# Optimization experiments

Hardware: AMD Instinct MI355X
Metric: run time of the kernel (lower is better)

Reference implementation:

```python
import jax, jax.numpy as jnp
import numpy as np

# spk_param = (thr, temp, damp); dt, tau from module config
THR, TEMP, DAMP = 0.4, 0.1, 0.9
DT, TAU = 0.1, 1.0


@jax.custom_vjp
def spike(v, u):
    # Stochastic Bernoulli spike: sigmoid(temp*v) > uniform noise
    return (jax.nn.sigmoid(TEMP * v) > u).astype(v.dtype)

def _spike_fwd(v, u):
    return spike(v, u), v

def _spike_bwd(v, g):
    # Faithful to the torch Spike.backward: returns the pseudo-derivative
    # damp*clamp(1-|v|,0) directly (the original ignores grad_output).
    return (DAMP * jnp.maximum(1.0 - jnp.abs(v), 0.0), jnp.zeros_like(v))

spike.defvjp(_spike_fwd, _spike_bwd)


def setup_inputs() -> dict:
    key = jax.random.key(0)
    k1, k2, k3, k4, k5 = jax.random.split(key, 5)
    B_, T, IN, N, OUT = 128, 512, 128, 512, 128
    inputs = jax.random.normal(k1, (B_, T, IN), dtype=jnp.float32)
    rand_u = jax.random.uniform(k2, (B_, T, N), dtype=jnp.float32)
    init_std = 1.0
    J = jax.random.normal(k3, (N, N), dtype=jnp.float32) * (init_std / np.sqrt(N))
    Bw = jax.random.normal(k4, (N, IN), dtype=jnp.float32)  # input projection (non-trainable in torch)
    W = jax.random.normal(k5, (OUT, N), dtype=jnp.float32) * (1.0 / np.sqrt(N))
    return {"inputs": inputs, "rand_u": rand_u, "J": J, "Bw": Bw, "W": W}


def reference(inputs, rand_u, J, Bw, W):
    B_, T, _ = inputs.shape
    N = J.shape[0]
    alpha = DT / TAU
    decay = 1.0 - alpha

    def step(carry, xs):
        v, z = carry
        x_t, u_t = xs  # [B, IN], [B, N]
        v_new = decay * v + alpha * z
        lamb = jnp.tanh(v_new) @ J.T + x_t @ Bw.T  # [B, N]
        z_new = spike((lamb - THR) / THR, u_t)
        out = lamb @ W.T  # [B, OUT]
        return (v_new, z_new), (v_new, z_new, out)

    v0 = jnp.zeros((B_, N), dtype=inputs.dtype)
    z0 = jnp.zeros((B_, N), dtype=inputs.dtype)
    xs = (jnp.swapaxes(inputs, 0, 1), jnp.swapaxes(rand_u, 0, 1))  # time-major
    _, (vs, zs, outs) = jax.lax.scan(step, (v0, z0), xs)

    vt = jnp.concatenate([v0[:, None, :], jnp.swapaxes(vs, 0, 1)], axis=1)  # [B, T+1, N]
    zt = jnp.concatenate([z0[:, None, :], jnp.swapaxes(zs, 0, 1)], axis=1)  # [B, T+1, N]
    output_seq = jnp.swapaxes(outs, 0, 1)  # [B, T, OUT]
    return vt, zt, output_seq
```

## Files before the change

### kernel.cpp

```cpp
#include <hip/hip_runtime.h>


typedef __attribute__((ext_vector_type(8))) short short8x;
typedef __attribute__((ext_vector_type(4))) float f32x4;

#define OFF_JQK  (0u)
#define OFF_BWH  (262144u)
#define OFF_BWL  (393216u)
#define OFF_G    (524288u)
#define OFF_M    (786432u)
#define OFF_GPK  (851968u)
#define OFF_MPK  (983040u)

#define SC_J 640.0f
#define SC_S 166.0f

__device__ __forceinline__ unsigned short f2bf(float f) {
  union { float f; unsigned u; } a; a.f = f;
  unsigned r = a.u + 0x7FFFu + ((a.u >> 16) & 1u);
  return (unsigned short)(r >> 16);
}
__device__ __forceinline__ float bf2f(unsigned short h) {
  union { unsigned u; float f; } a; a.u = ((unsigned)h) << 16;
  return a.f;
}
__device__ __forceinline__ float thr_of(float u) {
  return __builtin_fmaf(4.0f, __logf(u / (1.0f - u)), 0.4f);
}
__device__ __forceinline__ float fast_tanh_pos(float x) {
  const float e2 = __expf(x + x);
  return 1.0f - 2.0f / (e2 + 1.0f);
}
__device__ __forceinline__ int sdot4(unsigned a, unsigned b, int acc) {
#if __has_builtin(__builtin_amdgcn_sdot4)
  return __builtin_amdgcn_sdot4((int)a, (int)b, acc, false);
#else
  int r;
  asm("v_dot4_i32_i8 %0, %1, %2, %3" : "=v"(r) : "v"(a), "v"(b), "v"(acc));
  return r;
#endif
}
template <int CTRL>
__device__ __forceinline__ int dpp_add(int x) {
  return x + __builtin_amdgcn_update_dpp(0, x, CTRL, 0xF, 0xF, true);
}
__device__ __forceinline__ int dpp_reduce8(int x) {
  return dpp_add<0x141>(dpp_add<0x4E>(dpp_add<0xB1>(x)));
}

__launch_bounds__(512)
__global__ void jwm_kernel(const float* __restrict__ J, const float* __restrict__ Bw,
                           const float* __restrict__ W, unsigned char* __restrict__ ws) {
  __shared__ float wrow[512];
  const int o = blockIdx.x;
  const int tid = threadIdx.x;
  wrow[tid] = W[(size_t)o * 512 + tid];
  __syncthreads();
  const int k = tid, i = tid & 127;
  float g = 0.0f, m = 0.0f;
  for (int n = 0; n < 512; ++n) {
    const float wv = wrow[n];
    g = __builtin_fmaf(wv, J[(size_t)n * 512 + k], g);
    m = __builtin_fmaf(wv, Bw[(size_t)n * 128 + i], m);
  }
  ((float*)(ws + OFF_G))[(size_t)o * 512 + k] = g;
  if (tid < 128) ((float*)(ws + OFF_M))[(size_t)o * 128 + i] = m;
}

__global__ void pack_kernel(const float* __restrict__ J, const float* __restrict__ Bw,
                            unsigned char* __restrict__ ws) {
  const int id = blockIdx.x * 256 + threadIdx.x;
  if (id < 16384) {
    const int f = id;
    const int l = f & 63, j = (f >> 6) & 3, i = (f >> 8) & 7, w = f >> 11;
    const int kap = l & 7;
    const int n = w * 64 + (l >> 3) * 8 + i;
    const int k0 = 64 * kap + 16 * j;
    unsigned dw[4];
#pragma unroll
    for (int d = 0; d < 4; ++d) {
      unsigned x = 0;
#pragma unroll
      for (int p = 0; p < 4; ++p) {
        const float jv = J[(size_t)n * 512 + k0 + 4 * d + p];
        int q = __float2int_rn(jv * SC_J);
        q = q > 127 ? 127 : (q < -127 ? -127 : q);
        x |= ((unsigned)(q & 255)) << (8 * p);
      }
      dw[d] = x;
    }
    uint4 out; out.x = dw[0]; out.y = dw[1]; out.z = dw[2]; out.w = dw[3];
    ((uint4*)(ws + OFF_JQK))[f] = out;
  } else if (id < 24576) {
    const int idx = id - 16384;
    const int n = idx & 511, kg = idx >> 9, k0 = kg * 8;
    unsigned short* bwh = (unsigned short*)(ws + OFF_BWH);
    unsigned short* bwl = (unsigned short*)(ws + OFF_BWL);
    for (int e = 0; e < 8; ++e) {
      const float x = Bw[(size_t)n * 128 + k0 + e];
      const unsigned short h = f2bf(x);
      bwh[(size_t)idx * 8 + e] = h;
      bwl[(size_t)idx * 8 + e] = f2bf(x - bf2f(h));
    }
  } else if (id < 32768) {
    const int idx = id - 24576;
    const int o = idx & 127, kg = idx >> 7, k0 = kg * 8;
    const float* G = (const float*)(ws + OFF_G);
    unsigned short* gpk = (unsigned short*)(ws + OFF_GPK);
    for (int e = 0; e < 8; ++e) gpk[(size_t)idx * 8 + e] = f2bf(G[(size_t)o * 512 + k0 + e]);
  } else {
    const int idx = id - 32768;
    const int o = idx & 127, kg = idx >> 7, k0 = kg * 8;
    const float* M = (const float*)(ws + OFF_M);
    unsigned short* mpk = (unsigned short*)(ws + OFF_MPK);
    for (int e = 0; e < 8; ++e) mpk[(size_t)idx * 8 + e] = f2bf(M[(size_t)o * 128 + k0 + e]);
  }
}

__launch_bounds__(256)
__global__ void xpd_kernel(const float* __restrict__ X, const float* __restrict__ U,
                           const unsigned char* __restrict__ ws, float* __restrict__ Dbuf) {
  __shared__ short Ah[64 * 136];
  __shared__ short Al[64 * 136];
  const unsigned short* bwh = (const unsigned short*)(ws + OFF_BWH);
  const unsigned short* bwl = (const unsigned short*)(ws + OFF_BWL);
  const int m0 = blockIdx.x * 64;
  const int n0 = blockIdx.y * 64;
  const int tid = threadIdx.x;
  for (int i = tid; i < 64 * 32; i += 256) {
    const int r = i >> 5, kq = i & 31;
    const float4 x4 = *(const float4*)(X + (size_t)(m0 + r) * 128 + kq * 4);
    short4 h4, l4; unsigned short h;
    h = f2bf(x4.x); h4.x = (short)h; l4.x = (short)f2bf(x4.x - bf2f(h));
    h = f2bf(x4.y); h4.y = (short)h; l4.y = (short)f2bf(x4.y - bf2f(h));
    h = f2bf(x4.z); h4.z = (short)h; l4.z = (short)f2bf(x4.z - bf2f(h));
    h = f2bf(x4.w); h4.w = (short)h; l4.w = (short)f2bf(x4.w - bf2f(h));
    *(short4*)(&Ah[r * 136 + kq * 4]) = h4;
    *(short4*)(&Al[r * 136 + kq * 4]) = l4;
  }
  __syncthreads();
  const int w = tid >> 6, l = tid & 63, lhi = l >> 4, llo = l & 15;
  const int rowA = 16 * w + llo;
  f32x4 a0 = {0,0,0,0}, a1 = {0,0,0,0}, a2 = {0,0,0,0}, a3 = {0,0,0,0};
#pragma unroll
  for (int kt = 0; kt < 4; ++kt) {
    const short8x ah = *(const short8x*)(&Ah[rowA * 136 + kt * 32 + lhi * 8]);
    const short8x al = *(const short8x*)(&Al[rowA * 136 + kt * 32 + lhi * 8]);
#define XT(TI, ACC) { \
    const size_t bi = ((size_t)((kt * 4 + lhi) * 512 + n0 + TI * 16 + llo)) * 8; \
    const short8x bh = *(const short8x*)(bwh + bi); \
    const short8x bl = *(const short8x*)(bwl + bi); \
    ACC = __builtin_amdgcn_mfma_f32_16x16x32_bf16(ah, bh, ACC, 0, 0, 0); \
    ACC = __builtin_amdgcn_mfma_f32_16x16x32_bf16(al, bh, ACC, 0, 0, 0); \
    ACC = __builtin_amdgcn_mfma_f32_16x16x32_bf16(ah, bl, ACC, 0, 0, 0); }
    XT(0, a0) XT(1, a1) XT(2, a2) XT(3, a3)
#undef XT
  }
  const int n = n0 + llo;
#pragma unroll
  for (int r = 0; r < 4; ++r) {
    const int bt = m0 + 16 * w + lhi * 4 + r;
    const int bb = bt >> 9, tt = bt & 511;
    const float* urow = U + (size_t)bt * 512;
    float* drow = Dbuf + ((size_t)bb * 513 + tt + 1) * 512;
    drow[n]      = thr_of(urow[n])      - a0[r];
    drow[n + 16] = thr_of(urow[n + 16]) - a1[r];
    drow[n + 32] = thr_of(urow[n + 32]) - a2[r];
    drow[n + 48] = thr_of(urow[n + 48]) - a3[r];
  }
}

__launch_bounds__(512, 1)
__global__ void recur_kernel(const unsigned char* __restrict__ ws,
                             const float* __restrict__ Dv,
                             float* __restrict__ vtw, float* __restrict__ ztw) {
  __shared__ __align__(16) unsigned char s_sm[2][640];
  const int b = blockIdx.x;
  const int tid = threadIdx.x;
  const int w = tid >> 6, l = tid & 63;
  const int kap = l & 7, kap80 = kap * 80;

  uint4 jr[8][4];
#pragma unroll
  for (int i = 0; i < 8; ++i)
#pragma unroll
    for (int j = 0; j < 4; ++j) {
      const unsigned char* p = ws + OFF_JQK +
          (size_t)(((w * 8 + i) * 4 + j) * 64 + l) * 16;
      asm volatile("global_load_dwordx4 %0, %1, off" : "=v"(jr[i][j]) : "v"(p));
    }
  asm volatile("s_waitcnt vmcnt(0)" ::: "memory");

  const float SC = 1.0f / (SC_J * SC_S);
  vtw[((size_t)b * 513) * 512 + tid] = 0.0f;
  ztw[((size_t)b * 513) * 512 + tid] = 0.0f;

  const float* Dp = Dv + ((size_t)b * 513 + 1) * 512 + tid;
  float* vbase = vtw + ((size_t)b * 513 + 1) * 512 + tid;
  float* zbase = ztw + ((size_t)b * 513 + 1) * 512 + tid;

  float dc[8], dnx[8];
#pragma unroll
  for (int i = 0; i < 8; ++i) dc[i] = Dp[(size_t)i * 512];

  unsigned zprev = 0u;
  float v0 = 0.0f, v1 = 0.1f;
  unsigned q0 = (unsigned)__float2int_rn(fast_tanh_pos(v0) * SC_S);
  unsigned q1 = (unsigned)__float2int_rn(fast_tanh_pos(v1) * SC_S);

  for (int c = 0; c < 64; ++c) {
    const int t0 = c * 8;
#pragma unroll
    for (int i = 0; i < 8; ++i) dnx[i] = Dp[(size_t)(t0 + 8 + i) * 512];
    float v_arr[8];
    unsigned zbits = 0u;
#pragma unroll
    for (int i = 0; i < 8; ++i) {
      const int t = t0 + i;
      const unsigned q = zprev ? q1 : q0;
      const float v = zprev ? v1 : v0;
      v_arr[i] = v;
      s_sm[t & 1][w * 80 + l] = (unsigned char)q;
      asm volatile("s_waitcnt lgkmcnt(0)\n\ts_barrier" ::: "memory");
      v0 = 0.9f * v; v1 = v0 + 0.1f;
      q0 = (unsigned)__float2int_rn(fast_tanh_pos(v0) * SC_S);
      q1 = (unsigned)__float2int_rn(fast_tanh_pos(v1) * SC_S);
      const unsigned char* sb = &s_sm[t & 1][0];
      const uint4 s0 = *(const uint4*)(sb + kap80);
      const uint4 s1 = *(const uint4*)(sb + kap80 + 16);
      const uint4 s2 = *(const uint4*)(sb + kap80 + 32);
      const uint4 s3 = *(const uint4*)(sb + kap80 + 48);
      int a0 = 0, a1 = 0, a2 = 0, a3 = 0, a4 = 0, a5 = 0, a6 = 0, a7 = 0;
#define DOT(AI, I) \
      AI = sdot4(jr[I][0].x, s0.x, AI); AI = sdot4(jr[I][0].y, s0.y, AI); \
      AI = sdot4(jr[I][0].z, s0.z, AI); AI = sdot4(jr[I][0].w, s0.w, AI); \
      AI = sdot4(jr[I][1].x, s1.x, AI); AI = sdot4(jr[I][1].y, s1.y, AI); \
      AI = sdot4(jr[I][1].z, s1.z, AI); AI = sdot4(jr[I][1].w, s1.w, AI); \
      AI = sdot4(jr[I][2].x, s2.x, AI); AI = sdot4(jr[I][2].y, s2.y, AI); \
      AI = sdot4(jr[I][2].z, s2.z, AI); AI = sdot4(jr[I][2].w, s2.w, AI); \
      AI = sdot4(jr[I][3].x, s3.x, AI); AI = sdot4(jr[I][3].y, s3.y, AI); \
      AI = sdot4(jr[I][3].z, s3.z, AI); AI = sdot4(jr[I][3].w, s3.w, AI);
      DOT(a0, 0) DOT(a1, 1) DOT(a2, 2) DOT(a3, 3)
      DOT(a4, 4) DOT(a5, 5) DOT(a6, 6) DOT(a7, 7)
#undef DOT
      a0 = dpp_reduce8(a0); a1 = dpp_reduce8(a1);
      a2 = dpp_reduce8(a2); a3 = dpp_reduce8(a3);
      a4 = dpp_reduce8(a4); a5 = dpp_reduce8(a5);
      a6 = dpp_reduce8(a6); a7 = dpp_reduce8(a7);
      const int q01 = (l & 1) ? a1 : a0;
      const int q23 = (l & 1) ? a3 : a2;
      const int q45 = (l & 1) ? a5 : a4;
      const int q67 = (l & 1) ? a7 : a6;
      const int r0 = (l & 2) ? q23 : q01;
      const int r1 = (l & 2) ? q67 : q45;
      const int accv = (l & 4) ? r1 : r0;
      const float lam = (float)accv * SC;
      const unsigned z = (lam > dc[i]) ? 1u : 0u;
      zbits |= z << i;
      zprev = z;
    }
    unsigned zzero;
    asm("v_and_b32 %0, 0, %1" : "=v"(zzero) : "v"(zprev));
    float* vst = vbase + (size_t)t0 * 512 + zzero;
    float* zst = zbase + (size_t)t0 * 512;
#pragma unroll
    for (int i = 0; i < 8; ++i) {
      vst[(size_t)i * 512] = v_arr[i];
      zst[(size_t)i * 512] = ((zbits >> i) & 1u) ? 1.0f : 0.0f;
    }
#pragma unroll
    for (int i = 0; i < 8; ++i) dc[i] = dnx[i];
  }
}

__launch_bounds__(512)
__global__ void outk_kernel(const float* __restrict__ X, const float* __restrict__ vt,
                            const unsigned char* __restrict__ ws,
                            float* __restrict__ op) {
  __shared__ unsigned short sl[64 * 520];
  __shared__ unsigned short xl[64 * 136];
  const int m0 = blockIdx.x * 64;
  const int tid = threadIdx.x;
  const int w = tid >> 6, l = tid & 63, lhi = l >> 4, llo = l & 15;
  const unsigned short* gpk = (const unsigned short*)(ws + OFF_GPK);
  const unsigned short* mpk = (const unsigned short*)(ws + OFF_MPK);

#pragma unroll 4
  for (int r = 0; r < 64; ++r) {
    const int bt = m0 + r, b = bt >> 9, t = bt & 511;
    const float v = vt[((size_t)b * 513 + t + 1) * 512 + tid];
    sl[r * 520 + tid] = f2bf(fast_tanh_pos(v));
  }
#pragma unroll
  for (int i = 0; i < 16; ++i) {
    const int idx = i * 512 + tid;
    const int r = idx >> 7, c = idx & 127;
    const int bt = m0 + r;
    xl[r * 136 + c] = f2bf(X[(size_t)bt * 128 + c]);
  }
  __syncthreads();
  const int m = w >> 1, oh = (w & 1) * 4;
  f32x4 a0 = {0,0,0,0}, a1 = {0,0,0,0}, a2 = {0,0,0,0}, a3 = {0,0,0,0};
#pragma unroll
  for (int kt = 0; kt < 16; ++kt) {
    const short8x A = *(const short8x*)(sl + (m * 16 + llo) * 520 + kt * 32 + lhi * 8);
#define GT(TI, ACC) { \
    const short8x B = *(const short8x*)(gpk + ((size_t)((kt * 4 + lhi) * 128 + (oh + TI) * 16 + llo)) * 8); \
    ACC = __builtin_amdgcn_mfma_f32_16x16x32_bf16(A, B, ACC, 0, 0, 0); }
    GT(0, a0) GT(1, a1) GT(2, a2) GT(3, a3)
#undef GT
  }
#pragma unroll
  for (int kt = 0; kt < 4; ++kt) {
    const short8x A = *(const short8x*)(xl + (m * 16 + llo) * 136 + kt * 32 + lhi * 8);
#define MT(TI, ACC) { \
    const short8x B = *(const short8x*)(mpk + ((size_t)((kt * 4 + lhi) * 128 + (oh + TI) * 16 + llo)) * 8); \
    ACC = __builtin_amdgcn_mfma_f32_16x16x32_bf16(A, B, ACC, 0, 0, 0); }
    MT(0, a0) MT(1, a1) MT(2, a2) MT(3, a3)
#undef MT
  }
  float* obase = op + ((size_t)(m0 + m * 16 + lhi * 4)) * 128 + llo;
#pragma unroll
  for (int r = 0; r < 4; ++r) {
    float* orow = obase + (size_t)r * 128;
    orow[(oh + 0) * 16] = a0[r];
    orow[(oh + 1) * 16] = a1[r];
    orow[(oh + 2) * 16] = a2[r];
    orow[(oh + 3) * 16] = a3[r];
  }
}

extern "C" void kernel_launch(void* const* d_in, const int* in_sizes, int n_in,
                              void* d_out, int out_size, void* d_ws, size_t ws_size,
                              hipStream_t stream) {
  const float* X  = (const float*)d_in[0];
  const float* U  = (const float*)d_in[1];
  const float* J  = (const float*)d_in[2];
  const float* Bw = (const float*)d_in[3];
  const float* W  = (const float*)d_in[4];
  float* vt = (float*)d_out;
  float* zt = vt + (size_t)128 * 513 * 512;
  float* op = vt + (size_t)2 * 128 * 513 * 512;
  unsigned char* ws = (unsigned char*)d_ws;

  jwm_kernel<<<128, 512, 0, stream>>>(J, Bw, W, ws);
  pack_kernel<<<136, 256, 0, stream>>>(J, Bw, ws);
  xpd_kernel<<<dim3(1024, 8), 256, 0, stream>>>(X, U, ws, vt);
  recur_kernel<<<128, 512, 0, stream>>>(ws, vt, vt, zt);
  outk_kernel<<<1024, 512, 0, stream>>>(X, vt, ws, op);
}
```

Measured before the change: 680.5 us.

## Split recurrent int8 dot over 16 lanes with 1024-thread blocks

The recurrence kernel now runs 1024 threads per batch row instead of 512. Each neuron's J row is split across 16 lanes rather than 8, so each lane holds half the J registers and does half the sdot4 work per step, with an extra DPP stage in the reduction. The J packing layout is changed to match, duplicate lanes split the v and z stores between them, and next-step D loads are issued inline. The aim is to shorten the serial per-timestep critical path. The cost is a barrier across 16 waves instead of 8 and redundant spike computation in the duplicate lanes.

```diff
diff --git a/kernel.cpp b/kernel.cpp
--- a/kernel.cpp
+++ b/kernel.cpp
@@ -44,8 +44,8 @@
 __device__ __forceinline__ int dpp_add(int x) {
   return x + __builtin_amdgcn_update_dpp(0, x, CTRL, 0xF, 0xF, true);
 }
-__device__ __forceinline__ int dpp_reduce8(int x) {
-  return dpp_add<0x141>(dpp_add<0x4E>(dpp_add<0xB1>(x)));
+__device__ __forceinline__ int dpp_reduce16(int x) {
+  return dpp_add<0x140>(dpp_add<0x141>(dpp_add<0x4E>(dpp_add<0xB1>(x))));
 }
 
 __launch_bounds__(512)
@@ -72,10 +72,10 @@
   const int id = blockIdx.x * 256 + threadIdx.x;
   if (id < 16384) {
     const int f = id;
-    const int l = f & 63, j = (f >> 6) & 3, i = (f >> 8) & 7, w = f >> 11;
-    const int kap = l & 7;
-    const int n = w * 64 + (l >> 3) * 8 + i;
-    const int k0 = 64 * kap + 16 * j;
+    const int l = f & 63, j = (f >> 6) & 1, i = (f >> 7) & 7, w = f >> 10;
+    const int kap = l & 15;
+    const int n = w * 32 + (l >> 4) * 8 + i;
+    const int k0 = 32 * kap + 16 * j;
     unsigned dw[4];
 #pragma unroll
     for (int d = 0; d < 4; ++d) {
@@ -170,7 +170,7 @@
   }
 }
 
-__launch_bounds__(512, 1)
+__launch_bounds__(1024)
 __global__ void recur_kernel(const unsigned char* __restrict__ ws,
                              const float* __restrict__ Dv,
                              float* __restrict__ vtw, float* __restrict__ ztw) {
@@ -178,28 +178,33 @@
   const int b = blockIdx.x;
   const int tid = threadIdx.x;
   const int w = tid >> 6, l = tid & 63;
-  const int kap = l & 7, kap80 = kap * 80;
-
-  uint4 jr[8][4];
+  const int kap = l & 15;
+  const int n_own = w * 32 + (l >> 4) * 8 + (l & 7);
+  const int sm_wr = (n_own >> 6) * 80 + (n_own & 63);
+  const int roff = (kap >> 1) * 80 + (kap & 1) * 32;
+
+  uint4 jr[8][2];
 #pragma unroll
   for (int i = 0; i < 8; ++i)
 #pragma unroll
-    for (int j = 0; j < 4; ++j) {
+    for (int j = 0; j < 2; ++j) {
       const unsigned char* p = ws + OFF_JQK +
-          (size_t)(((w * 8 + i) * 4 + j) * 64 + l) * 16;
+          (size_t)(((w * 8 + i) * 2 + j) * 64 + l) * 16;
       asm volatile("global_load_dwordx4 %0, %1, off" : "=v"(jr[i][j]) : "v"(p));
     }
   asm volatile("s_waitcnt vmcnt(0)" ::: "memory");
 
   const float SC = 1.0f / (SC_J * SC_S);
-  vtw[((size_t)b * 513) * 512 + tid] = 0.0f;
-  ztw[((size_t)b * 513) * 512 + tid] = 0.0f;
-
-  const float* Dp = Dv + ((size_t)b * 513 + 1) * 512 + tid;
-  float* vbase = vtw + ((size_t)b * 513 + 1) * 512 + tid;
-  float* zbase = ztw + ((size_t)b * 513 + 1) * 512 + tid;
-
-  float dc[8], dnx[8];
+  if (tid < 512) {
+    vtw[((size_t)b * 513) * 512 + tid] = 0.0f;
+    ztw[((size_t)b * 513) * 512 + tid] = 0.0f;
+  }
+
+  const float* Dp = Dv + ((size_t)b * 513 + 1) * 512 + n_own;
+  float* vbase = vtw + ((size_t)b * 513 + 1) * 512 + n_own;
+  float* zbase = ztw + ((size_t)b * 513 + 1) * 512 + n_own;
+
+  float dc[8];
 #pragma unroll
   for (int i = 0; i < 8; ++i) dc[i] = Dp[(size_t)i * 512];
 
@@ -210,8 +215,6 @@
 
   for (int c = 0; c < 64; ++c) {
     const int t0 = c * 8;
-#pragma unroll
-    for (int i = 0; i < 8; ++i) dnx[i] = Dp[(size_t)(t0 + 8 + i) * 512];
     float v_arr[8];
     unsigned zbits = 0u;
 #pragma unroll
@@ -220,33 +223,27 @@
       const unsigned q = zprev ? q1 : q0;
       const float v = zprev ? v1 : v0;
       v_arr[i] = v;
-      s_sm[t & 1][w * 80 + l] = (unsigned char)q;
+      if (!(l & 8)) s_sm[t & 1][sm_wr] = (unsigned char)q;
       asm volatile("s_waitcnt lgkmcnt(0)\n\ts_barrier" ::: "memory");
       v0 = 0.9f * v; v1 = v0 + 0.1f;
       q0 = (unsigned)__float2int_rn(fast_tanh_pos(v0) * SC_S);
       q1 = (unsigned)__float2int_rn(fast_tanh_pos(v1) * SC_S);
       const unsigned char* sb = &s_sm[t & 1][0];
-      const uint4 s0 = *(const uint4*)(sb + kap80);
-      const uint4 s1 = *(const uint4*)(sb + kap80 + 16);
-      const uint4 s2 = *(const uint4*)(sb + kap80 + 32);
-      const uint4 s3 = *(const uint4*)(sb + kap80 + 48);
+      const uint4 s0 = *(const uint4*)(sb + roff);
+      const uint4 s1 = *(const uint4*)(sb + roff + 16);
       int a0 = 0, a1 = 0, a2 = 0, a3 = 0, a4 = 0, a5 = 0, a6 = 0, a7 = 0;
 #define DOT(AI, I) \
       AI = sdot4(jr[I][0].x, s0.x, AI); AI = sdot4(jr[I][0].y, s0.y, AI); \
       AI = sdot4(jr[I][0].z, s0.z, AI); AI = sdot4(jr[I][0].w, s0.w, AI); \
       AI = sdot4(jr[I][1].x, s1.x, AI); AI = sdot4(jr[I][1].y, s1.y, AI); \
-      AI = sdot4(jr[I][1].z, s1.z, AI); AI = sdot4(jr[I][1].w, s1.w, AI); \
-      AI = sdot4(jr[I][2].x, s2.x, AI); AI = sdot4(jr[I][2].y, s2.y, AI); \
-      AI = sdot4(jr[I][2].z, s2.z, AI); AI = sdot4(jr[I][2].w, s2.w, AI); \
-      AI = sdot4(jr[I][3].x, s3.x, AI); AI = sdot4(jr[I][3].y, s3.y, AI); \
-      AI = sdot4(jr[I][3].z, s3.z, AI); AI = sdot4(jr[I][3].w, s3.w, AI);
+      AI = sdot4(jr[I][1].z, s1.z, AI); AI = sdot4(jr[I][1].w, s1.w, AI);
       DOT(a0, 0) DOT(a1, 1) DOT(a2, 2) DOT(a3, 3)
       DOT(a4, 4) DOT(a5, 5) DOT(a6, 6) DOT(a7, 7)
 #undef DOT
-      a0 = dpp_reduce8(a0); a1 = dpp_reduce8(a1);
-      a2 = dpp_reduce8(a2); a3 = dpp_reduce8(a3);
-      a4 = dpp_reduce8(a4); a5 = dpp_reduce8(a5);
-      a6 = dpp_reduce8(a6); a7 = dpp_reduce8(a7);
+      a0 = dpp_reduce16(a0); a1 = dpp_reduce16(a1);
+      a2 = dpp_reduce16(a2); a3 = dpp_reduce16(a3);
+      a4 = dpp_reduce16(a4); a5 = dpp_reduce16(a5);
+      a6 = dpp_reduce16(a6); a7 = dpp_reduce16(a7);
       const int q01 = (l & 1) ? a1 : a0;
       const int q23 = (l & 1) ? a3 : a2;
       const int q45 = (l & 1) ? a5 : a4;
@@ -258,18 +255,19 @@
       const unsigned z = (lam > dc[i]) ? 1u : 0u;
       zbits |= z << i;
       zprev = z;
+      dc[i] = Dp[(size_t)(t0 + 8 + i) * 512];
     }
     unsigned zzero;
     asm("v_and_b32 %0, 0, %1" : "=v"(zzero) : "v"(zprev));
-    float* vst = vbase + (size_t)t0 * 512 + zzero;
-    float* zst = zbase + (size_t)t0 * 512;
-#pragma unroll
-    for (int i = 0; i < 8; ++i) {
-      vst[(size_t)i * 512] = v_arr[i];
-      zst[(size_t)i * 512] = ((zbits >> i) & 1u) ? 1.0f : 0.0f;
-    }
-#pragma unroll
-    for (int i = 0; i < 8; ++i) dc[i] = dnx[i];
+    if (!(l & 8)) {
+      float* vst = vbase + (size_t)t0 * 512 + zzero;
+#pragma unroll
+      for (int i = 0; i < 8; ++i) vst[(size_t)i * 512] = v_arr[i];
+    } else {
+      float* zst = zbase + (size_t)t0 * 512 + zzero;
+#pragma unroll
+      for (int i = 0; i < 8; ++i) zst[(size_t)i * 512] = ((zbits >> i) & 1u) ? 1.0f : 0.0f;
+    }
   }
 }
 
@@ -346,6 +344,6 @@
   jwm_kernel<<<128, 512, 0, stream>>>(J, Bw, W, ws);
   pack_kernel<<<136, 256, 0, stream>>>(J, Bw, ws);
   xpd_kernel<<<dim3(1024, 8), 256, 0, stream>>>(X, U, ws, vt);
-  recur_kernel<<<128, 512, 0, stream>>>(ws, vt, vt, zt);
+  recur_kernel<<<128, 1024, 0, stream>>>(ws, vt, vt, zt);
   outk_kernel<<<1024, 512, 0, stream>>>(X, vt, ws, op);
 }
```

New measurement: 892.3 us. 31.1% more time.

## Batch four sequences per block in recurrence using int8 MFMA matvec

Applied to the files above, without the earlier changes.

The recurrence kernel now handles four batch rows per block and computes the J·tanh(v) product with int8 MFMA 16x16x64 instructions instead of per-lane dot4 plus DPP reductions. J is repacked to match the MFMA operand layout, and results go through LDS so each thread can read its own neuron's lambda. This adds a second barrier per timestep, makes the grid only 32 blocks, and drops the precomputed two-branch tanh trick. The aim is more useful work per serial step, in exchange for fewer active CUs and more per-step synchronisation.

```diff
diff --git a/kernel.cpp b/kernel.cpp
--- a/kernel.cpp
+++ b/kernel.cpp
@@ -3,6 +3,7 @@
 
 typedef __attribute__((ext_vector_type(8))) short short8x;
 typedef __attribute__((ext_vector_type(4))) float f32x4;
+typedef __attribute__((ext_vector_type(4))) int i32x4;
 
 #define OFF_JQK  (0u)
 #define OFF_BWH  (262144u)
@@ -30,22 +31,6 @@
 __device__ __forceinline__ float fast_tanh_pos(float x) {
   const float e2 = __expf(x + x);
   return 1.0f - 2.0f / (e2 + 1.0f);
-}
-__device__ __forceinline__ int sdot4(unsigned a, unsigned b, int acc) {
-#if __has_builtin(__builtin_amdgcn_sdot4)
-  return __builtin_amdgcn_sdot4((int)a, (int)b, acc, false);
-#else
-  int r;
-  asm("v_dot4_i32_i8 %0, %1, %2, %3" : "=v"(r) : "v"(a), "v"(b), "v"(acc));
-  return r;
-#endif
-}
-template <int CTRL>
-__device__ __forceinline__ int dpp_add(int x) {
-  return x + __builtin_amdgcn_update_dpp(0, x, CTRL, 0xF, 0xF, true);
-}
-__device__ __forceinline__ int dpp_reduce8(int x) {
-  return dpp_add<0x141>(dpp_add<0x4E>(dpp_add<0xB1>(x)));
 }
 
 __launch_bounds__(512)
@@ -72,17 +57,16 @@
   const int id = blockIdx.x * 256 + threadIdx.x;
   if (id < 16384) {
     const int f = id;
-    const int l = f & 63, j = (f >> 6) & 3, i = (f >> 8) & 7, w = f >> 11;
-    const int kap = l & 7;
-    const int n = w * 64 + (l >> 3) * 8 + i;
-    const int k0 = 64 * kap + 16 * j;
+    const int l = f & 63, j = (f >> 6) & 7, m = (f >> 9) & 3, w = f >> 11;
+    const int row = w * 64 + m * 16 + (l & 15);
+    const int k0 = j * 64 + (l >> 4) * 16;
     unsigned dw[4];
 #pragma unroll
     for (int d = 0; d < 4; ++d) {
       unsigned x = 0;
 #pragma unroll
       for (int p = 0; p < 4; ++p) {
-        const float jv = J[(size_t)n * 512 + k0 + 4 * d + p];
+        const float jv = J[(size_t)row * 512 + k0 + 4 * d + p];
         int q = __float2int_rn(jv * SC_J);
         q = q > 127 ? 127 : (q < -127 ? -127 : q);
         x |= ((unsigned)(q & 255)) << (8 * p);
@@ -174,102 +158,96 @@
 __global__ void recur_kernel(const unsigned char* __restrict__ ws,
                              const float* __restrict__ Dv,
                              float* __restrict__ vtw, float* __restrict__ ztw) {
-  __shared__ __align__(16) unsigned char s_sm[2][640];
-  const int b = blockIdx.x;
+  __shared__ __align__(16) unsigned char sxb[4 * 544];
+  __shared__ __align__(16) int lam_s[4 * 552];
+  const int b0 = blockIdx.x * 4;
   const int tid = threadIdx.x;
   const int w = tid >> 6, l = tid & 63;
-  const int kap = l & 7, kap80 = kap * 80;
-
-  uint4 jr[8][4];
-#pragma unroll
-  for (int i = 0; i < 8; ++i)
-#pragma unroll
-    for (int j = 0; j < 4; ++j) {
+  const int q16 = l & 15, r4 = l >> 4;
+
+  i32x4 jr[4][8];
+#pragma unroll
+  for (int m = 0; m < 4; ++m)
+#pragma unroll
+    for (int j = 0; j < 8; ++j) {
       const unsigned char* p = ws + OFF_JQK +
-          (size_t)(((w * 8 + i) * 4 + j) * 64 + l) * 16;
-      asm volatile("global_load_dwordx4 %0, %1, off" : "=v"(jr[i][j]) : "v"(p));
+          (size_t)(((w * 4 + m) * 8 + j) * 64 + l) * 16;
+      asm volatile("global_load_dwordx4 %0, %1, off" : "=v"(jr[m][j]) : "v"(p));
     }
   asm volatile("s_waitcnt vmcnt(0)" ::: "memory");
 
   const float SC = 1.0f / (SC_J * SC_S);
-  vtw[((size_t)b * 513) * 512 + tid] = 0.0f;
-  ztw[((size_t)b * 513) * 512 + tid] = 0.0f;
-
-  const float* Dp = Dv + ((size_t)b * 513 + 1) * 512 + tid;
-  float* vbase = vtw + ((size_t)b * 513 + 1) * 512 + tid;
-  float* zbase = ztw + ((size_t)b * 513 + 1) * 512 + tid;
-
-  float dc[8], dnx[8];
-#pragma unroll
-  for (int i = 0; i < 8; ++i) dc[i] = Dp[(size_t)i * 512];
-
+#pragma unroll
+  for (int q = 0; q < 4; ++q) {
+    vtw[((size_t)(b0 + q) * 513) * 512 + tid] = 0.0f;
+    ztw[((size_t)(b0 + q) * 513) * 512 + tid] = 0.0f;
+  }
+
+  float dc[4][8];
+#pragma unroll
+  for (int q = 0; q < 4; ++q)
+#pragma unroll
+    for (int i = 0; i < 8; ++i)
+      dc[q][i] = Dv[((size_t)(b0 + q) * 513 + 1 + i) * 512 + tid];
+
+  float v[4] = {0.0f, 0.0f, 0.0f, 0.0f};
   unsigned zprev = 0u;
-  float v0 = 0.0f, v1 = 0.1f;
-  unsigned q0 = (unsigned)__float2int_rn(fast_tanh_pos(v0) * SC_S);
-  unsigned q1 = (unsigned)__float2int_rn(fast_tanh_pos(v1) * SC_S);
 
   for (int c = 0; c < 64; ++c) {
     const int t0 = c * 8;
-#pragma unroll
-    for (int i = 0; i < 8; ++i) dnx[i] = Dp[(size_t)(t0 + 8 + i) * 512];
-    float v_arr[8];
-    unsigned zbits = 0u;
+    float v_arr[4][8];
+    unsigned zbits[4] = {0u, 0u, 0u, 0u};
 #pragma unroll
     for (int i = 0; i < 8; ++i) {
-      const int t = t0 + i;
-      const unsigned q = zprev ? q1 : q0;
-      const float v = zprev ? v1 : v0;
-      v_arr[i] = v;
-      s_sm[t & 1][w * 80 + l] = (unsigned char)q;
+#pragma unroll
+      for (int q = 0; q < 4; ++q) {
+        const float add = ((zprev >> q) & 1u) ? 0.1f : 0.0f;
+        v[q] = __builtin_fmaf(0.9f, v[q], add);
+        v_arr[q][i] = v[q];
+        const float s = fast_tanh_pos(v[q]);
+        sxb[q * 544 + tid] = (unsigned char)__float2int_rn(s * SC_S);
+      }
       asm volatile("s_waitcnt lgkmcnt(0)\n\ts_barrier" ::: "memory");
-      v0 = 0.9f * v; v1 = v0 + 0.1f;
-      q0 = (unsigned)__float2int_rn(fast_tanh_pos(v0) * SC_S);
-      q1 = (unsigned)__float2int_rn(fast_tanh_pos(v1) * SC_S);
-      const unsigned char* sb = &s_sm[t & 1][0];
-      const uint4 s0 = *(const uint4*)(sb + kap80);
-      const uint4 s1 = *(const uint4*)(sb + kap80 + 16);
-      const uint4 s2 = *(const uint4*)(sb + kap80 + 32);
-      const uint4 s3 = *(const uint4*)(sb + kap80 + 48);
-      int a0 = 0, a1 = 0, a2 = 0, a3 = 0, a4 = 0, a5 = 0, a6 = 0, a7 = 0;
-#define DOT(AI, I) \
-      AI = sdot4(jr[I][0].x, s0.x, AI); AI = sdot4(jr[I][0].y, s0.y, AI); \
-      AI = sdot4(jr[I][0].z, s0.z, AI); AI = sdot4(jr[I][0].w, s0.w, AI); \
-      AI = sdot4(jr[I][1].x, s1.x, AI); AI = sdot4(jr[I][1].y, s1.y, AI); \
-      AI = sdot4(jr[I][1].z, s1.z, AI); AI = sdot4(jr[I][1].w, s1.w, AI); \
-      AI = sdot4(jr[I][2].x, s2.x, AI); AI = sdot4(jr[I][2].y, s2.y, AI); \
-      AI = sdot4(jr[I][2].z, s2.z, AI); AI = sdot4(jr[I][2].w, s2.w, AI); \
-      AI = sdot4(jr[I][3].x, s3.x, AI); AI = sdot4(jr[I][3].y, s3.y, AI); \
-      AI = sdot4(jr[I][3].z, s3.z, AI); AI = sdot4(jr[I][3].w, s3.w, AI);
-      DOT(a0, 0) DOT(a1, 1) DOT(a2, 2) DOT(a3, 3)
-      DOT(a4, 4) DOT(a5, 5) DOT(a6, 6) DOT(a7, 7)
-#undef DOT
-      a0 = dpp_reduce8(a0); a1 = dpp_reduce8(a1);
-      a2 = dpp_reduce8(a2); a3 = dpp_reduce8(a3);
-      a4 = dpp_reduce8(a4); a5 = dpp_reduce8(a5);
-      a6 = dpp_reduce8(a6); a7 = dpp_reduce8(a7);
-      const int q01 = (l & 1) ? a1 : a0;
-      const int q23 = (l & 1) ? a3 : a2;
-      const int q45 = (l & 1) ? a5 : a4;
-      const int q67 = (l & 1) ? a7 : a6;
-      const int r0 = (l & 2) ? q23 : q01;
-      const int r1 = (l & 2) ? q67 : q45;
-      const int accv = (l & 4) ? r1 : r0;
-      const float lam = (float)accv * SC;
-      const unsigned z = (lam > dc[i]) ? 1u : 0u;
-      zbits |= z << i;
-      zprev = z;
-    }
-    unsigned zzero;
-    asm("v_and_b32 %0, 0, %1" : "=v"(zzero) : "v"(zprev));
-    float* vst = vbase + (size_t)t0 * 512 + zzero;
-    float* zst = zbase + (size_t)t0 * 512;
-#pragma unroll
-    for (int i = 0; i < 8; ++i) {
-      vst[(size_t)i * 512] = v_arr[i];
-      zst[(size_t)i * 512] = ((zbits >> i) & 1u) ? 1.0f : 0.0f;
-    }
-#pragma unroll
-    for (int i = 0; i < 8; ++i) dc[i] = dnx[i];
+      i32x4 a0 = {0,0,0,0}, a1 = {0,0,0,0}, a2 = {0,0,0,0}, a3 = {0,0,0,0};
+#pragma unroll
+      for (int j = 0; j < 8; ++j) {
+        const i32x4 bf = *(const i32x4*)(sxb + (l & 3) * 544 + j * 64 + r4 * 16);
+        a0 = __builtin_amdgcn_mfma_i32_16x16x64_i8(jr[0][j], bf, a0, 0, 0, 0);
+        a1 = __builtin_amdgcn_mfma_i32_16x16x64_i8(jr[1][j], bf, a1, 0, 0, 0);
+        a2 = __builtin_amdgcn_mfma_i32_16x16x64_i8(jr[2][j], bf, a2, 0, 0, 0);
+        a3 = __builtin_amdgcn_mfma_i32_16x16x64_i8(jr[3][j], bf, a3, 0, 0, 0);
+      }
+      if (q16 < 4) {
+        const int nb = w * 64 + r4 * 4;
+        *(i32x4*)(lam_s + q16 * 552 + nb)      = a0;
+        *(i32x4*)(lam_s + q16 * 552 + nb + 16) = a1;
+        *(i32x4*)(lam_s + q16 * 552 + nb + 32) = a2;
+        *(i32x4*)(lam_s + q16 * 552 + nb + 48) = a3;
+      }
+      asm volatile("s_waitcnt lgkmcnt(0)\n\ts_barrier" ::: "memory");
+      unsigned znew = 0u;
+#pragma unroll
+      for (int q = 0; q < 4; ++q) {
+        const float lam = (float)lam_s[q * 552 + tid] * SC;
+        const unsigned zq = (lam > dc[q][i]) ? 1u : 0u;
+        znew |= zq << q;
+        zbits[q] |= zq << i;
+        dc[q][i] = Dv[((size_t)(b0 + q) * 513 + 1 + t0 + 8 + i) * 512 + tid];
+      }
+      zprev = znew;
+    }
+#pragma unroll
+    for (int q = 0; q < 4; ++q) {
+      unsigned zzero;
+      asm("v_and_b32 %0, 0, %1" : "=v"(zzero) : "v"(zbits[q]));
+      float* vst = vtw + ((size_t)(b0 + q) * 513 + 1 + t0) * 512 + tid + zzero;
+      float* zst = ztw + ((size_t)(b0 + q) * 513 + 1 + t0) * 512 + tid;
+#pragma unroll
+      for (int i = 0; i < 8; ++i) {
+        vst[(size_t)i * 512] = v_arr[q][i];
+        zst[(size_t)i * 512] = ((zbits[q] >> i) & 1u) ? 1.0f : 0.0f;
+      }
+    }
   }
 }
 
@@ -346,6 +324,6 @@
   jwm_kernel<<<128, 512, 0, stream>>>(J, Bw, W, ws);
   pack_kernel<<<136, 256, 0, stream>>>(J, Bw, ws);
   xpd_kernel<<<dim3(1024, 8), 256, 0, stream>>>(X, U, ws, vt);
-  recur_kernel<<<128, 512, 0, stream>>>(ws, vt, vt, zt);
+  recur_kernel<<<32, 512, 0, stream>>>(ws, vt, vt, zt);
   outk_kernel<<<1024, 512, 0, stream>>>(X, vt, ws, op);
 }
```

Result: slower. 916.3 us (+34.6%).

## Fuse output projection into recurrence tail and pack G/M in jwm

Applied to the files above, without the earlier changes.

The separate output-projection kernel is removed. Its work now runs at the end of the recurrence kernel: each batch block walks its 512 timesteps in chunks of 64, applies tanh to its own v values, converts them to bf16 in shared memory and runs the same MFMA GEMM against G and M. The jwm kernel now writes G and M directly in packed bf16 layout, so the fp32 intermediates and two branches of pack_kernel go away. This saves a launch and an intermediate buffer round trip. The cost is that the output GEMM now runs on only 128 blocks, serially over 8 chunks, instead of 1024 blocks, and it adds about 83KB of shared memory to the recurrence kernel.

```diff
diff --git a/kernel.cpp b/kernel.cpp
--- a/kernel.cpp
+++ b/kernel.cpp
@@ -7,8 +7,6 @@
 #define OFF_JQK  (0u)
 #define OFF_BWH  (262144u)
 #define OFF_BWL  (393216u)
-#define OFF_G    (524288u)
-#define OFF_M    (786432u)
 #define OFF_GPK  (851968u)
 #define OFF_MPK  (983040u)
 
@@ -63,8 +61,12 @@
     g = __builtin_fmaf(wv, J[(size_t)n * 512 + k], g);
     m = __builtin_fmaf(wv, Bw[(size_t)n * 128 + i], m);
   }
-  ((float*)(ws + OFF_G))[(size_t)o * 512 + k] = g;
-  if (tid < 128) ((float*)(ws + OFF_M))[(size_t)o * 128 + i] = m;
+  unsigned short* gpk = (unsigned short*)(ws + OFF_GPK);
+  gpk[((size_t)(((k >> 5) * 4 + ((k >> 3) & 3)) * 128 + o)) * 8 + (k & 7)] = f2bf(g);
+  if (tid < 128) {
+    unsigned short* mpk = (unsigned short*)(ws + OFF_MPK);
+    mpk[((size_t)(((i >> 5) * 4 + ((i >> 3) & 3)) * 128 + o)) * 8 + (i & 7)] = f2bf(m);
+  }
 }
 
 __global__ void pack_kernel(const float* __restrict__ J, const float* __restrict__ Bw,
@@ -91,7 +93,7 @@
     }
     uint4 out; out.x = dw[0]; out.y = dw[1]; out.z = dw[2]; out.w = dw[3];
     ((uint4*)(ws + OFF_JQK))[f] = out;
-  } else if (id < 24576) {
+  } else {
     const int idx = id - 16384;
     const int n = idx & 511, kg = idx >> 9, k0 = kg * 8;
     unsigned short* bwh = (unsigned short*)(ws + OFF_BWH);
@@ -102,18 +104,6 @@
       bwh[(size_t)idx * 8 + e] = h;
       bwl[(size_t)idx * 8 + e] = f2bf(x - bf2f(h));
     }
-  } else if (id < 32768) {
-    const int idx = id - 24576;
-    const int o = idx & 127, kg = idx >> 7, k0 = kg * 8;
-    const float* G = (const float*)(ws + OFF_G);
-    unsigned short* gpk = (unsigned short*)(ws + OFF_GPK);
-    for (int e = 0; e < 8; ++e) gpk[(size_t)idx * 8 + e] = f2bf(G[(size_t)o * 512 + k0 + e]);
-  } else {
-    const int idx = id - 32768;
-    const int o = idx & 127, kg = idx >> 7, k0 = kg * 8;
-    const float* M = (const float*)(ws + OFF_M);
-    unsigned short* mpk = (unsigned short*)(ws + OFF_MPK);
-    for (int e = 0; e < 8; ++e) mpk[(size_t)idx * 8 + e] = f2bf(M[(size_t)o * 128 + k0 + e]);
   }
 }
 
@@ -173,8 +163,11 @@
 __launch_bounds__(512, 1)
 __global__ void recur_kernel(const unsigned char* __restrict__ ws,
                              const float* __restrict__ Dv,
-                             float* __restrict__ vtw, float* __restrict__ ztw) {
+                             float* __restrict__ vtw, float* __restrict__ ztw,
+                             const float* __restrict__ X, float* __restrict__ op) {
   __shared__ __align__(16) unsigned char s_sm[2][640];
+  __shared__ unsigned short sl[64 * 520];
+  __shared__ unsigned short xl[64 * 136];
   const int b = blockIdx.x;
   const int tid = threadIdx.x;
   const int w = tid >> 6, l = tid & 63;
@@ -271,62 +264,55 @@
 #pragma unroll
     for (int i = 0; i < 8; ++i) dc[i] = dnx[i];
   }
-}
-
-__launch_bounds__(512)
-__global__ void outk_kernel(const float* __restrict__ X, const float* __restrict__ vt,
-                            const unsigned char* __restrict__ ws,
-                            float* __restrict__ op) {
-  __shared__ unsigned short sl[64 * 520];
-  __shared__ unsigned short xl[64 * 136];
-  const int m0 = blockIdx.x * 64;
-  const int tid = threadIdx.x;
-  const int w = tid >> 6, l = tid & 63, lhi = l >> 4, llo = l & 15;
-  const unsigned short* gpk = (const unsigned short*)(ws + OFF_GPK);
-  const unsigned short* mpk = (const unsigned short*)(ws + OFF_MPK);
-
-#pragma unroll 4
-  for (int r = 0; r < 64; ++r) {
-    const int bt = m0 + r, b = bt >> 9, t = bt & 511;
-    const float v = vt[((size_t)b * 513 + t + 1) * 512 + tid];
-    sl[r * 520 + tid] = f2bf(fast_tanh_pos(v));
-  }
-#pragma unroll
-  for (int i = 0; i < 16; ++i) {
-    const int idx = i * 512 + tid;
-    const int r = idx >> 7, c = idx & 127;
-    const int bt = m0 + r;
-    xl[r * 136 + c] = f2bf(X[(size_t)bt * 128 + c]);
-  }
-  __syncthreads();
-  const int m = w >> 1, oh = (w & 1) * 4;
-  f32x4 a0 = {0,0,0,0}, a1 = {0,0,0,0}, a2 = {0,0,0,0}, a3 = {0,0,0,0};
-#pragma unroll
-  for (int kt = 0; kt < 16; ++kt) {
-    const short8x A = *(const short8x*)(sl + (m * 16 + llo) * 520 + kt * 32 + lhi * 8);
+
+  asm volatile("s_waitcnt vmcnt(0)" ::: "memory");
+  {
+    const unsigned short* gpk = (const unsigned short*)(ws + OFF_GPK);
+    const unsigned short* mpk = (const unsigned short*)(ws + OFF_MPK);
+    const int lhi = l >> 4, llo = l & 15;
+    const int m = w >> 1, oh = (w & 1) * 4;
+    for (int c2 = 0; c2 < 8; ++c2) {
+      const float* vrd = vtw + ((size_t)b * 513 + c2 * 64 + 1) * 512 + tid;
+#pragma unroll 8
+      for (int r = 0; r < 64; ++r)
+        sl[r * 520 + tid] = f2bf(fast_tanh_pos(vrd[(size_t)r * 512]));
+#pragma unroll
+      for (int i2 = 0; i2 < 16; ++i2) {
+        const int idx = i2 * 512 + tid;
+        const int r = idx >> 7, cc = idx & 127;
+        xl[r * 136 + cc] = f2bf(X[((size_t)b * 512 + c2 * 64 + r) * 128 + cc]);
+      }
+      __syncthreads();
+      f32x4 a0 = {0,0,0,0}, a1 = {0,0,0,0}, a2 = {0,0,0,0}, a3 = {0,0,0,0};
+#pragma unroll
+      for (int kt = 0; kt < 16; ++kt) {
+        const short8x A = *(const short8x*)(sl + (m * 16 + llo) * 520 + kt * 32 + lhi * 8);
 #define GT(TI, ACC) { \
-    const short8x B = *(const short8x*)(gpk + ((size_t)((kt * 4 + lhi) * 128 + (oh + TI) * 16 + llo)) * 8); \
-    ACC = __builtin_amdgcn_mfma_f32_16x16x32_bf16(A, B, ACC, 0, 0, 0); }
-    GT(0, a0) GT(1, a1) GT(2, a2) GT(3, a3)
+        const short8x B = *(const short8x*)(gpk + ((size_t)((kt * 4 + lhi) * 128 + (oh + TI) * 16 + llo)) * 8); \
+        ACC = __builtin_amdgcn_mfma_f32_16x16x32_bf16(A, B, ACC, 0, 0, 0); }
+        GT(0, a0) GT(1, a1) GT(2, a2) GT(3, a3)
 #undef GT
-  }
-#pragma unroll
-  for (int kt = 0; kt < 4; ++kt) {
-    const short8x A = *(const short8x*)(xl + (m * 16 + llo) * 136 + kt * 32 + lhi * 8);
+      }
+#pragma unroll
+      for (int kt = 0; kt < 4; ++kt) {
+        const short8x A = *(const short8x*)(xl + (m * 16 + llo) * 136 + kt * 32 + lhi * 8);
 #define MT(TI, ACC) { \
-    const short8x B = *(const short8x*)(mpk + ((size_t)((kt * 4 + lhi) * 128 + (oh + TI) * 16 + llo)) * 8); \
-    ACC = __builtin_amdgcn_mfma_f32_16x16x32_bf16(A, B, ACC, 0, 0, 0); }
-    MT(0, a0) MT(1, a1) MT(2, a2) MT(3, a3)
+        const short8x B = *(const short8x*)(mpk + ((size_t)((kt * 4 + lhi) * 128 + (oh + TI) * 16 + llo)) * 8); \
+        ACC = __builtin_amdgcn_mfma_f32_16x16x32_bf16(A, B, ACC, 0, 0, 0); }
+        MT(0, a0) MT(1, a1) MT(2, a2) MT(3, a3)
 #undef MT
-  }
-  float* obase = op + ((size_t)(m0 + m * 16 + lhi * 4)) * 128 + llo;
-#pragma unroll
-  for (int r = 0; r < 4; ++r) {
-    float* orow = obase + (size_t)r * 128;
-    orow[(oh + 0) * 16] = a0[r];
-    orow[(oh + 1) * 16] = a1[r];
-    orow[(oh + 2) * 16] = a2[r];
-    orow[(oh + 3) * 16] = a3[r];
+      }
+      float* obase = op + ((size_t)b * 512 + c2 * 64 + m * 16 + lhi * 4) * 128 + llo;
+#pragma unroll
+      for (int r = 0; r < 4; ++r) {
+        float* orow = obase + (size_t)r * 128;
+        orow[(oh + 0) * 16] = a0[r];
+        orow[(oh + 1) * 16] = a1[r];
+        orow[(oh + 2) * 16] = a2[r];
+        orow[(oh + 3) * 16] = a3[r];
+      }
+      __syncthreads();
+    }
   }
 }
 
@@ -344,8 +330,7 @@
   unsigned char* ws = (unsigned char*)d_ws;
 
   jwm_kernel<<<128, 512, 0, stream>>>(J, Bw, W, ws);
-  pack_kernel<<<136, 256, 0, stream>>>(J, Bw, ws);
+  pack_kernel<<<96, 256, 0, stream>>>(J, Bw, ws);
   xpd_kernel<<<dim3(1024, 8), 256, 0, stream>>>(X, U, ws, vt);
-  recur_kernel<<<128, 512, 0, stream>>>(ws, vt, vt, zt);
-  outk_kernel<<<1024, 512, 0, stream>>>(X, vt, ws, op);
-}
+  recur_kernel<<<128, 512, 0, stream>>>(ws, vt, vt, zt, X, op);
+}
```

After: 706.0 us. +3.7%, slower.
